# Optimization experiments

Measured on AMD Instinct MI355X. Metric: run time of the kernel, lower is better.

The kernel has to match this reference:

```python
import jax, jax.numpy as jnp
import numpy as np

N = 50000        # nodes
E = 800000       # edges (before self-loops)
F_IN = 128       # input features
HID = 32         # per-head hidden channels
H1 = 4           # heads of conv1
H2 = 8           # heads of conv2
NEG_SLOPE = 0.2  # PyG GATConv LeakyReLU slope
E_DEC = 100000   # pos/neg decode edges each


def setup_inputs() -> dict:
    key = jax.random.key(0)
    ks = jax.random.split(key, 12)
    s = 0.1
    return {
        "x": jax.random.normal(ks[0], (N, F_IN), jnp.float32),
        "edge_index": jax.random.randint(ks[1], (2, E), 0, N, dtype=jnp.int32),
        "pos_edge_index": jax.random.randint(ks[2], (2, E_DEC), 0, N, dtype=jnp.int32),
        "neg_edge_index": jax.random.randint(ks[3], (2, E_DEC), 0, N, dtype=jnp.int32),
        "W1": jax.random.normal(ks[4], (F_IN, H1 * HID), jnp.float32) * s,
        "a_src1": jax.random.normal(ks[5], (H1, HID), jnp.float32) * s,
        "a_dst1": jax.random.normal(ks[6], (H1, HID), jnp.float32) * s,
        "b1": jax.random.normal(ks[7], (H1 * HID,), jnp.float32) * s,
        "W2": jax.random.normal(ks[8], (H1 * HID, H2 * HID), jnp.float32) * s,
        "a_src2": jax.random.normal(ks[9], (H2, HID), jnp.float32) * s,
        "a_dst2": jax.random.normal(ks[10], (H2, HID), jnp.float32) * s,
        "b2": jax.random.normal(ks[11], (H2 * HID,), jnp.float32) * s,
    }


def _segment_softmax(e, seg, n):
    # softmax over edges grouped by destination node; max is detached (cancels analytically)
    m = jax.lax.stop_gradient(jax.ops.segment_max(e, seg, num_segments=n))
    ex = jnp.exp(e - m[seg])
    denom = jax.ops.segment_sum(ex, seg, num_segments=n)
    return ex / (denom[seg] + 1e-16)


def _gat_conv(x, src, dst, W, a_src, a_dst, b, heads, out_ch):
    n = x.shape[0]
    h = (x @ W).reshape(n, heads, out_ch)             # [N,H,C]
    al_s = (h * a_src[None]).sum(-1)                  # [N,H]
    al_d = (h * a_dst[None]).sum(-1)                  # [N,H]
    e = al_s[src] + al_d[dst]                         # [E,H] edge logits
    e = jnp.where(e > 0, e, NEG_SLOPE * e)            # LeakyReLU
    alpha = _segment_softmax(e, dst, n)               # [E,H]
    msg = h[src] * alpha[:, :, None]                  # [E,H,C]
    out = jax.ops.segment_sum(msg, dst, num_segments=n)  # [N,H,C]
    return out.reshape(n, heads * out_ch) + b


def reference(x, edge_index, pos_edge_index, neg_edge_index,
              W1, a_src1, a_dst1, b1, W2, a_src2, a_dst2, b2):
    n = x.shape[0]
    loops = jnp.arange(n, dtype=edge_index.dtype)     # PyG add_self_loops=True
    src = jnp.concatenate([edge_index[0], loops])
    dst = jnp.concatenate([edge_index[1], loops])
    # encode
    z = jax.nn.relu(_gat_conv(x, src, dst, W1, a_src1, a_dst1, b1, H1, HID))
    z = _gat_conv(z, src, dst, W2, a_src2, a_dst2, b2, H2, HID)
    # decode
    ei = jnp.concatenate([pos_edge_index, neg_edge_index], axis=1)
    logits = (z[ei[0]] * z[ei[1]]).sum(-1)            # [2*E_DEC]
    return logits
```

## Files before the change

kernel.cpp:

```cpp
#include <hip/hip_runtime.h>
#include <hip/hip_bf16.h>

#define NN 50000
#define EE 800000
#define ET (EE + NN)
#define F_IN 128
#define HID 32
#define H1 4
#define H2 8
#define E_DEC 100000
#define NEG_SLOPE 0.2f

typedef __attribute__((ext_vector_type(8))) short short8;
typedef __attribute__((ext_vector_type(4))) float floatx4;

__device__ __forceinline__ unsigned short f2b(float f) {
    __hip_bfloat16 h = __float2bfloat16(f);
    return *reinterpret_cast<unsigned short*>(&h);
}
__device__ __forceinline__ float b2f(unsigned short u) {
    return __uint_as_float(((unsigned int)u) << 16);
}

__global__ void fillint_k(int* __restrict__ p, int n) {
    int i = blockIdx.x * blockDim.x + threadIdx.x;
    if (i < n) p[i] = 0;
}

__global__ void hist_k(const int* __restrict__ ei, int* __restrict__ counts) {
    int e = blockIdx.x * blockDim.x + threadIdx.x;
    if (e >= ET) return;
    int d = (e < EE) ? ei[EE + e] : e - EE;
    atomicAdd(&counts[d], 1);
}

__global__ void scan1_k(const int* __restrict__ counts, int* __restrict__ bsum) {
    __shared__ int sh[256];
    int t = threadIdx.x;
    int i = blockIdx.x * 256 + t;
    sh[t] = (i < NN) ? counts[i] : 0;
    __syncthreads();
    for (int off = 128; off > 0; off >>= 1) {
        if (t < off) sh[t] += sh[t + off];
        __syncthreads();
    }
    if (t == 0) bsum[blockIdx.x] = sh[0];
}

__global__ void scan2_k(int* __restrict__ bsum, int nb, int* __restrict__ start) {
    __shared__ int sh[256];
    int t = threadIdx.x;
    int v = (t < nb) ? bsum[t] : 0;
    sh[t] = v;
    __syncthreads();
    for (int off = 1; off < 256; off <<= 1) {
        int u = (t >= off) ? sh[t - off] : 0;
        __syncthreads();
        sh[t] += u;
        __syncthreads();
    }
    if (t < nb) bsum[t] = sh[t] - v;
    if (t == 0) start[NN] = ET;
}

__global__ void scan3_k(const int* __restrict__ counts, const int* __restrict__ bsum,
                        int* __restrict__ start, int* __restrict__ cursor) {
    __shared__ int sh[256];
    int t = threadIdx.x;
    int i = blockIdx.x * 256 + t;
    int c = (i < NN) ? counts[i] : 0;
    sh[t] = c;
    __syncthreads();
    for (int off = 1; off < 256; off <<= 1) {
        int u = (t >= off) ? sh[t - off] : 0;
        __syncthreads();
        sh[t] += u;
        __syncthreads();
    }
    int excl = sh[t] - c + bsum[blockIdx.x];
    if (i < NN) {
        start[i] = excl;
        cursor[i] = excl;
    }
}

__global__ void scatter_k(const int* __restrict__ ei, int* __restrict__ cursor,
                          int* __restrict__ csr) {
    int e = blockIdx.x * blockDim.x + threadIdx.x;
    if (e >= ET) return;
    int s, d;
    if (e < EE) { s = ei[e]; d = ei[EE + e]; } else { s = d = e - EE; }
    int slot = atomicAdd(&cursor[d], 1);
    csr[slot] = s;
}

__global__ void cvt_k(const float4* __restrict__ X, ushort4* __restrict__ Xb, int n4) {
    int i = blockIdx.x * blockDim.x + threadIdx.x;
    if (i >= n4) return;
    float4 v = X[i];
    ushort4 o;
    o.x = f2b(v.x);
    o.y = f2b(v.y);
    o.z = f2b(v.z);
    o.w = f2b(v.w);
    Xb[i] = o;
}

template <int OUT>
__global__ void packW_k(const float* __restrict__ W, unsigned short* __restrict__ Wp) {
    const int total = (OUT / 16) * 4 * 64;
    int id = blockIdx.x * 256 + threadIdx.x;
    if (id >= total) return;
    const int col = ((id >> 8) << 4) + (id & 15);
    const int k0 = ((id >> 6) & 3) * 32 + ((id >> 4) & 3) * 8;
    ushort4 lo, hi;
    lo.x = f2b(W[(k0 + 0) * OUT + col]);
    lo.y = f2b(W[(k0 + 1) * OUT + col]);
    lo.z = f2b(W[(k0 + 2) * OUT + col]);
    lo.w = f2b(W[(k0 + 3) * OUT + col]);
    hi.x = f2b(W[(k0 + 4) * OUT + col]);
    hi.y = f2b(W[(k0 + 5) * OUT + col]);
    hi.z = f2b(W[(k0 + 6) * OUT + col]);
    hi.w = f2b(W[(k0 + 7) * OUT + col]);
    ((ushort4*)Wp)[id * 2] = lo;
    ((ushort4*)Wp)[id * 2 + 1] = hi;
}

template <int OUT, int CT>
__global__ void mfma_gemm_k(const unsigned short* __restrict__ Xb,
                            const unsigned short* __restrict__ Wp,
                            unsigned short* __restrict__ Hout) {
    const int wave = threadIdx.x >> 6;
    const int lane = threadIdx.x & 63;
    const int quad = lane >> 4;
    const int rl = lane & 15;
    const int r0 = blockIdx.x * 64;
    floatx4 acc[4][CT];
#pragma unroll
    for (int rt = 0; rt < 4; ++rt)
#pragma unroll
        for (int ct = 0; ct < CT; ++ct) acc[rt][ct] = {0.f, 0.f, 0.f, 0.f};

#pragma unroll
    for (int ks = 0; ks < 4; ++ks) {
        short8 a[4];
#pragma unroll
        for (int rt = 0; rt < 4; ++rt) {
            int row = r0 + rt * 16 + rl;
            row = row < NN ? row : NN - 1;
            a[rt] = *(const short8*)(Xb + (long long)row * 128 + ks * 32 + quad * 8);
        }
#pragma unroll
        for (int ct = 0; ct < CT; ++ct) {
            const int ctg = wave * CT + ct;
            const short8 b = *(const short8*)(Wp + (((ctg * 4 + ks) * 64 + lane) << 3));
#pragma unroll
            for (int rt = 0; rt < 4; ++rt)
                acc[rt][ct] = __builtin_amdgcn_mfma_f32_16x16x32_bf16(a[rt], b, acc[rt][ct], 0, 0, 0);
        }
    }
#pragma unroll
    for (int rt = 0; rt < 4; ++rt) {
        const int rowbase = r0 + rt * 16 + quad * 4;
#pragma unroll
        for (int ct = 0; ct < CT; ++ct) {
            const int col = (wave * CT + ct) * 16 + rl;
#pragma unroll
            for (int r = 0; r < 4; ++r) {
                const int row = rowbase + r;
                if (row < NN) Hout[(long long)row * OUT + col] = f2b(acc[rt][ct][r]);
            }
        }
    }
}

template <int OUT, int H>
__global__ void al_k(const unsigned short* __restrict__ Hb, const float* __restrict__ a_src,
                     const float* __restrict__ a_dst, float* __restrict__ als,
                     float* __restrict__ ald) {
    const int wave = threadIdx.x >> 6;
    const int lane = threadIdx.x & 63;
    const int row = blockIdx.x * 4 + wave;
    const int CPL = OUT / 64;
    const int G = 32 / CPL;
    const int c0 = lane * CPL;
    const int hd = c0 >> 5;
    float ps = 0.f, pd = 0.f;
#pragma unroll
    for (int j = 0; j < CPL; ++j) {
        const float hv = b2f(Hb[(long long)row * OUT + c0 + j]);
        const int cc = hd * 32 + ((c0 + j) & 31);
        ps += hv * a_src[cc];
        pd += hv * a_dst[cc];
    }
#pragma unroll
    for (int m = G / 2; m >= 1; m >>= 1) {
        ps += __shfl_xor(ps, m, 64);
        pd += __shfl_xor(pd, m, 64);
    }
    if ((lane & (G - 1)) == 0) {
        als[row * H + hd] = ps;
        ald[row * H + hd] = pd;
    }
}

template <int OUT, int H, bool RELU>
__global__ void gather_k(const int* __restrict__ start, const int* __restrict__ csr,
                         const float* __restrict__ als, const float* __restrict__ ald,
                         const unsigned short* __restrict__ Hin,
                         const float* __restrict__ bias, unsigned short* __restrict__ outp) {
    constexpr int LPR = OUT / 4;
    constexpr int EPW = 64 / LPR;
    const int d = blockIdx.x;
    const int lane = threadIdx.x;
    const int cl = lane & (LPR - 1);
    const int slot = lane >> (LPR == 64 ? 6 : 5);
    const int hd = cl >> 3;
    const int beg = start[d], end = start[d + 1];
    const float aldd = ald[d * H + hd];
    float a0 = 0.f, a1 = 0.f, a2 = 0.f, a3 = 0.f, den = 0.f;
    int i = beg + slot;
    for (; i + 3 * EPW < end; i += 4 * EPW) {
        const int s0 = csr[i], s1 = csr[i + EPW], s2 = csr[i + 2 * EPW], s3 = csr[i + 3 * EPW];
        float l0 = als[s0 * H + hd] + aldd;
        float l1 = als[s1 * H + hd] + aldd;
        float l2 = als[s2 * H + hd] + aldd;
        float l3 = als[s3 * H + hd] + aldd;
        const ushort4 h0 = *(const ushort4*)(Hin + (long long)s0 * OUT + cl * 4);
        const ushort4 h1 = *(const ushort4*)(Hin + (long long)s1 * OUT + cl * 4);
        const ushort4 h2 = *(const ushort4*)(Hin + (long long)s2 * OUT + cl * 4);
        const ushort4 h3 = *(const ushort4*)(Hin + (long long)s3 * OUT + cl * 4);
        l0 = l0 > 0.f ? l0 : NEG_SLOPE * l0;
        l1 = l1 > 0.f ? l1 : NEG_SLOPE * l1;
        l2 = l2 > 0.f ? l2 : NEG_SLOPE * l2;
        l3 = l3 > 0.f ? l3 : NEG_SLOPE * l3;
        const float w0 = __expf(l0), w1 = __expf(l1), w2 = __expf(l2), w3 = __expf(l3);
        den += (w0 + w1) + (w2 + w3);
        a0 += w0 * b2f(h0.x) + w1 * b2f(h1.x) + w2 * b2f(h2.x) + w3 * b2f(h3.x);
        a1 += w0 * b2f(h0.y) + w1 * b2f(h1.y) + w2 * b2f(h2.y) + w3 * b2f(h3.y);
        a2 += w0 * b2f(h0.z) + w1 * b2f(h1.z) + w2 * b2f(h2.z) + w3 * b2f(h3.z);
        a3 += w0 * b2f(h0.w) + w1 * b2f(h1.w) + w2 * b2f(h2.w) + w3 * b2f(h3.w);
    }
    for (; i < end; i += EPW) {
        const int s = csr[i];
        float lg = als[s * H + hd] + aldd;
        lg = lg > 0.f ? lg : NEG_SLOPE * lg;
        const float w = __expf(lg);
        const ushort4 hv = *(const ushort4*)(Hin + (long long)s * OUT + cl * 4);
        den += w;
        a0 += w * b2f(hv.x);
        a1 += w * b2f(hv.y);
        a2 += w * b2f(hv.z);
        a3 += w * b2f(hv.w);
    }
    if (EPW == 2) {
        a0 += __shfl_xor(a0, 32, 64);
        a1 += __shfl_xor(a1, 32, 64);
        a2 += __shfl_xor(a2, 32, 64);
        a3 += __shfl_xor(a3, 32, 64);
        den += __shfl_xor(den, 32, 64);
    }
    if (lane < LPR) {
        const float inv = 1.f / (den + 1e-16f);
        const int c0 = cl * 4;
        float v0 = a0 * inv + bias[c0];
        float v1 = a1 * inv + bias[c0 + 1];
        float v2 = a2 * inv + bias[c0 + 2];
        float v3 = a3 * inv + bias[c0 + 3];
        if (RELU) {
            v0 = v0 > 0.f ? v0 : 0.f;
            v1 = v1 > 0.f ? v1 : 0.f;
            v2 = v2 > 0.f ? v2 : 0.f;
            v3 = v3 > 0.f ? v3 : 0.f;
        }
        ushort4 o;
        o.x = f2b(v0);
        o.y = f2b(v1);
        o.z = f2b(v2);
        o.w = f2b(v3);
        *(ushort4*)(outp + (long long)d * OUT + c0) = o;
    }
}

__global__ void decode_k(const int* __restrict__ pei, const int* __restrict__ nei,
                         const unsigned short* __restrict__ z2, float* __restrict__ out) {
    const int w = threadIdx.x >> 6, lane = threadIdx.x & 63;
    const int idx = blockIdx.x * 4 + w;
    if (idx >= 2 * E_DEC) return;
    int a, b;
    if (idx < E_DEC) {
        a = pei[idx];
        b = pei[E_DEC + idx];
    } else {
        const int j = idx - E_DEC;
        a = nei[j];
        b = nei[E_DEC + j];
    }
    const ushort4 ua = *(const ushort4*)(z2 + (long long)a * 256 + lane * 4);
    const ushort4 ub = *(const ushort4*)(z2 + (long long)b * 256 + lane * 4);
    float s = b2f(ua.x) * b2f(ub.x) + b2f(ua.y) * b2f(ub.y) +
              b2f(ua.z) * b2f(ub.z) + b2f(ua.w) * b2f(ub.w);
#pragma unroll
    for (int m = 32; m >= 1; m >>= 1) s += __shfl_xor(s, m, 64);
    if (lane == 0) out[idx] = s;
}

extern "C" void kernel_launch(void* const* d_in, const int* in_sizes, int n_in,
                              void* d_out, int out_size, void* d_ws, size_t ws_size,
                              hipStream_t stream) {
    const float* x = (const float*)d_in[0];
    const int* ei = (const int*)d_in[1];
    const int* pei = (const int*)d_in[2];
    const int* nei = (const int*)d_in[3];
    const float* W1 = (const float*)d_in[4];
    const float* as1 = (const float*)d_in[5];
    const float* ad1 = (const float*)d_in[6];
    const float* b1 = (const float*)d_in[7];
    const float* W2 = (const float*)d_in[8];
    const float* as2 = (const float*)d_in[9];
    const float* ad2 = (const float*)d_in[10];
    const float* b2 = (const float*)d_in[11];
    float* out = (float*)d_out;

    unsigned short* h1 = (unsigned short*)d_ws;
    unsigned short* h2 = h1 + (long long)NN * 128;
    unsigned short* z2 = h2 + (long long)NN * 256;
    unsigned short* z1 = z2 + (long long)NN * 256;
    unsigned short* xb = z1 + (long long)NN * 128;
    unsigned short* wp1 = xb + (long long)NN * 128;
    unsigned short* wp2 = wp1 + 128 * 128;
    float* als1 = (float*)(wp2 + 128 * 256);
    float* ald1 = als1 + NN * H1;
    float* als2 = ald1 + NN * H1;
    float* ald2 = als2 + NN * H2;
    int* counts = (int*)(ald2 + NN * H2);
    int* start = counts + NN;
    int* cursor = start + NN + 1;
    int* bsum = cursor + NN;
    int* csr = bsum + 256;

    const int NB = (NN + 255) / 256;

    fillint_k<<<NB, 256, 0, stream>>>(counts, NN);
    hist_k<<<(ET + 255) / 256, 256, 0, stream>>>(ei, counts);
    scan1_k<<<NB, 256, 0, stream>>>(counts, bsum);
    scan2_k<<<1, 256, 0, stream>>>(bsum, NB, start);
    scan3_k<<<NB, 256, 0, stream>>>(counts, bsum, start, cursor);
    scatter_k<<<(ET + 255) / 256, 256, 0, stream>>>(ei, cursor, csr);

    const int n4 = NN * 128 / 4;
    cvt_k<<<(n4 + 255) / 256, 256, 0, stream>>>((const float4*)x, (ushort4*)xb, n4);
    packW_k<128><<<(2048 + 255) / 256, 256, 0, stream>>>(W1, wp1);
    packW_k<256><<<(4096 + 255) / 256, 256, 0, stream>>>(W2, wp2);

    mfma_gemm_k<128, 2><<<(NN + 63) / 64, 256, 0, stream>>>(xb, wp1, h1);
    al_k<128, H1><<<NN / 4, 256, 0, stream>>>(h1, as1, ad1, als1, ald1);
    gather_k<128, H1, true><<<NN, 64, 0, stream>>>(start, csr, als1, ald1, h1, b1, z1);

    mfma_gemm_k<256, 4><<<(NN + 63) / 64, 256, 0, stream>>>(z1, wp2, h2);
    al_k<256, H2><<<NN / 4, 256, 0, stream>>>(h2, as2, ad2, als2, ald2);
    gather_k<256, H2, false><<<NN, 64, 0, stream>>>(start, csr, als2, ald2, h2, b2, z2);

    decode_k<<<(2 * E_DEC + 3) / 4, 256, 0, stream>>>(pei, nei, z2, out);
}
```

Baseline: 383.0 us.

## Fuse fp32-to-bf16 conversion and attention-logit computation into the MFMA GEMM

Drops the separate fp32-to-bf16 conversion kernel: the first GEMM now reads fp32 x directly and converts it in registers. The per-node attention dot products (al_s, al_d) are computed in the GEMM epilogue from the fp32 accumulators using cross-lane shuffles, which removes the al_k kernels and their re-read of H. This cuts two kernel launches plus extra memory passes per layer. In exchange the GEMM loads twice the bytes for A in layer 1 and does more epilogue shuffle work, and the logits now come from fp32 accumulators instead of bf16-rounded values, which changes numerics slightly.

```diff
diff --git a/kernel.cpp b/kernel.cpp
--- a/kernel.cpp
+++ b/kernel.cpp
@@ -92,18 +92,6 @@
     if (e < EE) { s = ei[e]; d = ei[EE + e]; } else { s = d = e - EE; }
     int slot = atomicAdd(&cursor[d], 1);
     csr[slot] = s;
-}
-
-__global__ void cvt_k(const float4* __restrict__ X, ushort4* __restrict__ Xb, int n4) {
-    int i = blockIdx.x * blockDim.x + threadIdx.x;
-    if (i >= n4) return;
-    float4 v = X[i];
-    ushort4 o;
-    o.x = f2b(v.x);
-    o.y = f2b(v.y);
-    o.z = f2b(v.z);
-    o.w = f2b(v.w);
-    Xb[i] = o;
 }
 
 template <int OUT>
@@ -126,10 +114,12 @@
     ((ushort4*)Wp)[id * 2 + 1] = hi;
 }
 
-template <int OUT, int CT>
-__global__ void mfma_gemm_k(const unsigned short* __restrict__ Xb,
+template <int OUT, int H, int CT, bool F32IN>
+__global__ void mfma_gemm_k(const void* __restrict__ Xin,
                             const unsigned short* __restrict__ Wp,
-                            unsigned short* __restrict__ Hout) {
+                            const float* __restrict__ a_src, const float* __restrict__ a_dst,
+                            unsigned short* __restrict__ Hout,
+                            float* __restrict__ als, float* __restrict__ ald) {
     const int wave = threadIdx.x >> 6;
     const int lane = threadIdx.x & 63;
     const int quad = lane >> 4;
@@ -148,7 +138,25 @@
         for (int rt = 0; rt < 4; ++rt) {
             int row = r0 + rt * 16 + rl;
             row = row < NN ? row : NN - 1;
-            a[rt] = *(const short8*)(Xb + (long long)row * 128 + ks * 32 + quad * 8);
+            if (F32IN) {
+                const float4* xp =
+                    (const float4*)((const float*)Xin + (long long)row * 128 + ks * 32 + quad * 8);
+                const float4 v0 = xp[0];
+                const float4 v1 = xp[1];
+                short8 t;
+                t[0] = (short)f2b(v0.x);
+                t[1] = (short)f2b(v0.y);
+                t[2] = (short)f2b(v0.z);
+                t[3] = (short)f2b(v0.w);
+                t[4] = (short)f2b(v1.x);
+                t[5] = (short)f2b(v1.y);
+                t[6] = (short)f2b(v1.z);
+                t[7] = (short)f2b(v1.w);
+                a[rt] = t;
+            } else {
+                a[rt] = *(const short8*)((const unsigned short*)Xin +
+                                         (long long)row * 128 + ks * 32 + quad * 8);
+            }
         }
 #pragma unroll
         for (int ct = 0; ct < CT; ++ct) {
@@ -172,35 +180,38 @@
             }
         }
     }
-}
-
-template <int OUT, int H>
-__global__ void al_k(const unsigned short* __restrict__ Hb, const float* __restrict__ a_src,
-                     const float* __restrict__ a_dst, float* __restrict__ als,
-                     float* __restrict__ ald) {
-    const int wave = threadIdx.x >> 6;
-    const int lane = threadIdx.x & 63;
-    const int row = blockIdx.x * 4 + wave;
-    const int CPL = OUT / 64;
-    const int G = 32 / CPL;
-    const int c0 = lane * CPL;
-    const int hd = c0 >> 5;
-    float ps = 0.f, pd = 0.f;
-#pragma unroll
-    for (int j = 0; j < CPL; ++j) {
-        const float hv = b2f(Hb[(long long)row * OUT + c0 + j]);
-        const int cc = hd * 32 + ((c0 + j) & 31);
-        ps += hv * a_src[cc];
-        pd += hv * a_dst[cc];
-    }
-#pragma unroll
-    for (int m = G / 2; m >= 1; m >>= 1) {
-        ps += __shfl_xor(ps, m, 64);
-        pd += __shfl_xor(pd, m, 64);
-    }
-    if ((lane & (G - 1)) == 0) {
-        als[row * H + hd] = ps;
-        ald[row * H + hd] = pd;
+    float asv[CT], adv[CT];
+#pragma unroll
+    for (int ct = 0; ct < CT; ++ct) {
+        const int col = (wave * CT + ct) * 16 + rl;
+        asv[ct] = a_src[col];
+        adv[ct] = a_dst[col];
+    }
+#pragma unroll
+    for (int rt = 0; rt < 4; ++rt) {
+#pragma unroll
+        for (int r = 0; r < 4; ++r) {
+            const int row = r0 + rt * 16 + quad * 4 + r;
+            float ps[CT / 2], pd[CT / 2];
+#pragma unroll
+            for (int hh = 0; hh < CT / 2; ++hh) {
+                ps[hh] = acc[rt][2 * hh][r] * asv[2 * hh] + acc[rt][2 * hh + 1][r] * asv[2 * hh + 1];
+                pd[hh] = acc[rt][2 * hh][r] * adv[2 * hh] + acc[rt][2 * hh + 1][r] * adv[2 * hh + 1];
+#pragma unroll
+                for (int m = 8; m >= 1; m >>= 1) {
+                    ps[hh] += __shfl_xor(ps[hh], m, 64);
+                    pd[hh] += __shfl_xor(pd[hh], m, 64);
+                }
+            }
+            if (rl == 0 && row < NN) {
+#pragma unroll
+                for (int hh = 0; hh < CT / 2; ++hh) {
+                    const int hd = wave * (CT / 2) + hh;
+                    als[row * H + hd] = ps[hh];
+                    ald[row * H + hd] = pd[hh];
+                }
+            }
+        }
     }
 }
 
@@ -326,8 +337,7 @@
     unsigned short* h2 = h1 + (long long)NN * 128;
     unsigned short* z2 = h2 + (long long)NN * 256;
     unsigned short* z1 = z2 + (long long)NN * 256;
-    unsigned short* xb = z1 + (long long)NN * 128;
-    unsigned short* wp1 = xb + (long long)NN * 128;
+    unsigned short* wp1 = z1 + (long long)NN * 128;
     unsigned short* wp2 = wp1 + 128 * 128;
     float* als1 = (float*)(wp2 + 128 * 256);
     float* ald1 = als1 + NN * H1;
@@ -348,17 +358,15 @@
     scan3_k<<<NB, 256, 0, stream>>>(counts, bsum, start, cursor);
     scatter_k<<<(ET + 255) / 256, 256, 0, stream>>>(ei, cursor, csr);
 
-    const int n4 = NN * 128 / 4;
-    cvt_k<<<(n4 + 255) / 256, 256, 0, stream>>>((const float4*)x, (ushort4*)xb, n4);
     packW_k<128><<<(2048 + 255) / 256, 256, 0, stream>>>(W1, wp1);
     packW_k<256><<<(4096 + 255) / 256, 256, 0, stream>>>(W2, wp2);
 
-    mfma_gemm_k<128, 2><<<(NN + 63) / 64, 256, 0, stream>>>(xb, wp1, h1);
-    al_k<128, H1><<<NN / 4, 256, 0, stream>>>(h1, as1, ad1, als1, ald1);
+    mfma_gemm_k<128, H1, 2, true><<<(NN + 63) / 64, 256, 0, stream>>>(
+        x, wp1, as1, ad1, h1, als1, ald1);
     gather_k<128, H1, true><<<NN, 64, 0, stream>>>(start, csr, als1, ald1, h1, b1, z1);
 
-    mfma_gemm_k<256, 4><<<(NN + 63) / 64, 256, 0, stream>>>(z1, wp2, h2);
-    al_k<256, H2><<<NN / 4, 256, 0, stream>>>(h2, as2, ad2, als2, ald2);
+    mfma_gemm_k<256, H2, 4, false><<<(NN + 63) / 64, 256, 0, stream>>>(
+        z1, wp2, as2, ad2, h2, als2, ald2);
     gather_k<256, H2, false><<<NN, 64, 0, stream>>>(start, csr, als2, ald2, h2, b2, z2);
 
     decode_k<<<(2 * E_DEC + 3) / 4, 256, 0, stream>>>(pei, nei, z2, out);
```

New measurement: 380.4 us. About the same (-0.7%).
